# Performance work log

Hardware: AMD Instinct MI355X
Metric: run time of the kernel (lower is better)

The kernel has to match this reference:

```python
import jax, jax.numpy as jnp
import numpy as np

B, L, D = 2, 2048, 1024
H = 16
HD = D // H  # 64


def _orthogonal_projection(key, d, m):
    g = jax.random.normal(key, (d, m), dtype=jnp.float32)
    q, r = jnp.linalg.qr(g)
    s = jnp.sign(jnp.diagonal(r))
    s = jnp.where(s == 0, 1.0, s)
    q = q * s[None, :]
    # preserve_variance=True
    return q * np.sqrt(d / m)


def setup_inputs() -> dict:
    key = jax.random.key(0)
    ks = jax.random.split(key, 8)
    x = jax.random.normal(ks[0], (B, L, D), dtype=jnp.float32)
    p = jax.random.normal(ks[1], (B, L, D), dtype=jnp.float32)
    s = 1.0 / np.sqrt(D)
    W_qkv = jax.random.uniform(ks[2], (3 * D, D), dtype=jnp.float32, minval=-s, maxval=s)
    b_qkv = jax.random.uniform(ks[3], (3 * D,), dtype=jnp.float32, minval=-s, maxval=s)
    W_out = jax.random.uniform(ks[4], (D, D), dtype=jnp.float32, minval=-s, maxval=s)
    b_out = jax.random.uniform(ks[5], (D,), dtype=jnp.float32, minval=-s, maxval=s)
    proj = _orthogonal_projection(ks[6], D, D // 2)
    return {"x": x, "p": p, "W_qkv": W_qkv, "b_qkv": b_qkv,
            "W_out": W_out, "b_out": b_out, "proj": proj}


def reference(x, p, W_qkv, b_qkv, W_out, b_out, proj):
    # QKV projection: (B,L,D) -> (B,L,3,H,HD)
    qkv = (jnp.einsum('bld,ed->ble', x, W_qkv) + b_qkv).reshape(B, L, 3, H, HD)
    q, k, v = qkv[:, :, 0], qkv[:, :, 1], qkv[:, :, 2]

    # Collaborative rotary phases from conditioning tokens: (B,L,H,HD/2)
    phases = (p @ proj).reshape(B, L, H, HD // 2)  # phase_scale = 1.0
    cos, sin = jnp.cos(phases), jnp.sin(phases)

    half = HD // 2
    # non-interleaved rotary: split head_dim into two halves
    def rot(t):
        t1, t2 = t[..., :half], t[..., half:]
        return jnp.concatenate([t1 * cos - t2 * sin, t1 * sin + t2 * cos], axis=-1)

    q, k = rot(q), rot(k)

    scale = HD ** -0.5
    scores = jnp.einsum('bqhd,bkhd->bhqk', q, k) * scale
    attn = jax.nn.softmax(scores, axis=-1)
    out = jnp.einsum('bhqk,bkhd->bqhd', attn, v).reshape(B, L, D)
    return jnp.einsum('bld,ed->ble', out, W_out) + b_out
```

## Files before the change

kernel.cpp:

```cpp
#include <hip/hip_runtime.h>
#include <hip/hip_bf16.h>
#include <math.h>

namespace {
constexpr int Bb = 2;
constexpr int Ll = 2048;
constexpr int Dd = 1024;
constexpr int Hh = 16;
constexpr int NT = Bb * Ll;
constexpr int D3 = 3 * Dd;
constexpr int PH = Dd / 2;
constexpr int LDK = 72;
}

typedef __attribute__((ext_vector_type(8))) short bf16x8;
typedef __attribute__((ext_vector_type(4))) short bf16x4;
typedef __attribute__((ext_vector_type(4))) float f32x4;

#if defined(__has_builtin)
#if __has_builtin(__builtin_amdgcn_mfma_f32_16x16x16bf16_1k)
#define HAVE_MFMA16 1
#endif
#endif

__device__ inline unsigned pack2bf(float a, float b) {
  __hip_bfloat162 t = __float22bfloat162_rn(float2{a, b});
  union { __hip_bfloat162 h; unsigned u; } cv; cv.h = t;
  return cv.u;
}

__device__ inline bf16x4 u2bf4(uint2 u) {
  union { uint2 u; bf16x4 v; } c; c.u = u; return c.v;
}

__device__ inline f32x4 pv_mfma(bf16x4 va, bf16x4 vb, f32x4 c) {
#ifdef HAVE_MFMA16
  return __builtin_amdgcn_mfma_f32_16x16x16bf16_1k(va, vb, c, 0, 0, 0);
#else
  const bf16x8 a8 = {va[0], va[1], va[2], va[3], 0, 0, 0, 0};
  const bf16x8 b8 = {vb[0], vb[1], vb[2], vb[3], 0, 0, 0, 0};
  return __builtin_amdgcn_mfma_f32_16x16x32_bf16(a8, b8, c, 0, 0, 0);
#endif
}

__device__ inline void async_cp16(const void* gsrc, void* ldst) {
  __builtin_amdgcn_global_load_lds(
      (const __attribute__((address_space(1))) unsigned int*)gsrc,
      (__attribute__((address_space(3))) unsigned int*)ldst, 16, 0, 0);
}

__global__ __launch_bounds__(256) void cast3_kernel(
    const float4* __restrict__ x, const float4* __restrict__ wq,
    const float4* __restrict__ wo,
    uint2* __restrict__ xd, uint2* __restrict__ wqd, uint2* __restrict__ wod)
{
  int i = blockIdx.x * 256 + threadIdx.x;
  const float4* s; uint2* d;
  if (i < 1048576) { s = x; d = xd; }
  else if (i < 1048576 + 786432) { i -= 1048576; s = wq; d = wqd; }
  else { i -= 1048576 + 786432; s = wo; d = wod; }
  const float4 f = s[i];
  d[i] = make_uint2(pack2bf(f.x, f.y), pack2bf(f.z, f.w));
}

__global__ __launch_bounds__(256) void split_cast_kernel(
    const float4* __restrict__ src, uint2* __restrict__ hi, uint2* __restrict__ lo, int n4)
{
  const int i = blockIdx.x * 256 + threadIdx.x;
  if (i >= n4) return;
  const float4 f = src[i];
  float hf[4], lf[4];
  const float ff[4] = {f.x, f.y, f.z, f.w};
#pragma unroll
  for (int j = 0; j < 4; ++j) {
    const __hip_bfloat16 h = __float2bfloat16(ff[j]);
    hf[j] = __bfloat162float(h);
    lf[j] = ff[j] - hf[j];
  }
  hi[i] = make_uint2(pack2bf(hf[0], hf[1]), pack2bf(hf[2], hf[3]));
  lo[i] = make_uint2(pack2bf(lf[0], lf[1]), pack2bf(lf[2], lf[3]));
}

__global__ __launch_bounds__(256) void trans_split_kernel(
    const float* __restrict__ proj, short* __restrict__ th, short* __restrict__ tl)
{
  __shared__ float Ls[64][65];
  const int tid = threadIdx.x;
  const int d0 = blockIdx.x * 64, m0 = blockIdx.y * 64;
  const int r = tid >> 4, c4 = (tid & 15) * 4;
#pragma unroll
  for (int it = 0; it < 4; ++it) {
    const int row = it * 16 + r;
    const float4 v = *(const float4*)&proj[(size_t)(d0 + row) * PH + m0 + c4];
    Ls[row][c4] = v.x; Ls[row][c4+1] = v.y; Ls[row][c4+2] = v.z; Ls[row][c4+3] = v.w;
  }
  __syncthreads();
#pragma unroll
  for (int it = 0; it < 4; ++it) {
    const int row = it * 16 + r;
    float hf[4], lf[4];
#pragma unroll
    for (int j = 0; j < 4; ++j) {
      const float v = Ls[c4 + j][row];
      const __hip_bfloat16 h = __float2bfloat16(v);
      hf[j] = __bfloat162float(h);
      lf[j] = v - hf[j];
    }
    *(uint2*)&th[(size_t)(m0 + row) * Dd + d0 + c4] = make_uint2(pack2bf(hf[0], hf[1]), pack2bf(hf[2], hf[3]));
    *(uint2*)&tl[(size_t)(m0 + row) * Dd + d0 + c4] = make_uint2(pack2bf(lf[0], lf[1]), pack2bf(lf[2], lf[3]));
  }
}

__global__ __launch_bounds__(256) void gemm_nn_split(
    const short* __restrict__ Ah_g, const short* __restrict__ Al_g,
    const short* __restrict__ Wh_g, const short* __restrict__ Wl_g,
    float* __restrict__ C)
{
  __shared__ __align__(16) short Ah[64 * 32], Al[64 * 32], Wh[64 * 32], Wl[64 * 32];
  const int tid = threadIdx.x;
  const int w = tid >> 6, lane = tid & 63;
  const int l15 = lane & 15, quad = lane >> 4;
  const int wn = w >> 1, wm = w & 1;
  const int n0 = blockIdx.y * 64, m0 = blockIdx.x * 64;

  const int row = tid >> 2, cc = tid & 3;
  const int ksw = (cc ^ (row & 3)) * 8;
  const short* gAh = Ah_g + (size_t)(n0 + row) * Dd + ksw;
  const short* gAl = Al_g + (size_t)(n0 + row) * Dd + ksw;
  const short* gWh = Wh_g + (size_t)(m0 + row) * Dd + ksw;
  const short* gWl = Wl_g + (size_t)(m0 + row) * Dd + ksw;
  short* lAh = Ah + tid * 8;
  short* lAl = Al + tid * 8;
  short* lWh = Wh + tid * 8;
  short* lWl = Wl + tid * 8;

  f32x4 acc[2][2];
#pragma unroll
  for (int i = 0; i < 2; ++i)
#pragma unroll
    for (int j = 0; j < 2; ++j) acc[i][j] = f32x4{0.f, 0.f, 0.f, 0.f};

  const int swq = (quad ^ (l15 & 3)) * 8;

  for (int k0 = 0; k0 < Dd; k0 += 32) {
    __syncthreads();
    async_cp16(gAh + k0, lAh);
    async_cp16(gAl + k0, lAl);
    async_cp16(gWh + k0, lWh);
    async_cp16(gWl + k0, lWl);
    __syncthreads();

    bf16x8 ah[2], al[2], wh[2], wl[2];
#pragma unroll
    for (int i = 0; i < 2; ++i) {
      ah[i] = *(const bf16x8*)&Ah[(wn * 32 + i * 16 + l15) * 32 + swq];
      al[i] = *(const bf16x8*)&Al[(wn * 32 + i * 16 + l15) * 32 + swq];
    }
#pragma unroll
    for (int j = 0; j < 2; ++j) {
      wh[j] = *(const bf16x8*)&Wh[(wm * 32 + j * 16 + l15) * 32 + swq];
      wl[j] = *(const bf16x8*)&Wl[(wm * 32 + j * 16 + l15) * 32 + swq];
    }
#pragma unroll
    for (int i = 0; i < 2; ++i)
#pragma unroll
      for (int j = 0; j < 2; ++j) {
        acc[i][j] = __builtin_amdgcn_mfma_f32_16x16x32_bf16(ah[i], wh[j], acc[i][j], 0, 0, 0);
        acc[i][j] = __builtin_amdgcn_mfma_f32_16x16x32_bf16(ah[i], wl[j], acc[i][j], 0, 0, 0);
        acc[i][j] = __builtin_amdgcn_mfma_f32_16x16x32_bf16(al[i], wh[j], acc[i][j], 0, 0, 0);
      }
  }

#pragma unroll
  for (int i = 0; i < 2; ++i)
#pragma unroll
    for (int r = 0; r < 4; ++r) {
      float* crow = C + (size_t)(n0 + wn * 32 + i * 16 + quad * 4 + r) * PH + m0 + wm * 32 + l15;
#pragma unroll
      for (int j = 0; j < 2; ++j) crow[j * 16] = acc[i][j][r];
    }
}

__global__ __launch_bounds__(256) void gemm_qkv_fused(
    const __hip_bfloat16* __restrict__ A, const __hip_bfloat16* __restrict__ W,
    const float* __restrict__ bias, const float* __restrict__ phases,
    __hip_bfloat16* __restrict__ q_bf, __hip_bfloat16* __restrict__ k_bf,
    __hip_bfloat16* __restrict__ vt_g)
{
  __shared__ __align__(16) short As[128 * 32];
  __shared__ __align__(16) short Ws[128 * 32];
  const int tid = threadIdx.x;
  const int w = tid >> 6, lane = tid & 63;
  const int l15 = lane & 15, quad = lane >> 4;
  const int wn = w >> 1, wm = w & 1;
  const int n0 = blockIdx.y * 128, m0 = blockIdx.x * 128;

  const int row = tid >> 2, cc = tid & 3;
  const int ksw = (cc ^ (row & 3)) * 8;
  const short* gA  = (const short*)A + (size_t)(n0 + row) * Dd + ksw;
  const short* gW  = (const short*)W + (size_t)(m0 + row) * Dd + ksw;
  short* lA  = As + tid * 8;
  short* lA2 = As + 2048 + tid * 8;
  short* lW  = Ws + tid * 8;
  short* lW2 = Ws + 2048 + tid * 8;

  f32x4 acc[4][4];
#pragma unroll
  for (int i = 0; i < 4; ++i)
#pragma unroll
    for (int j = 0; j < 4; ++j) acc[i][j] = f32x4{0.f, 0.f, 0.f, 0.f};

  const int swq = (quad ^ (l15 & 3)) * 8;

  for (int k0 = 0; k0 < Dd; k0 += 32) {
    __syncthreads();
    async_cp16(gA + k0, lA);
    async_cp16(gA + 64 * Dd + k0, lA2);
    async_cp16(gW + k0, lW);
    async_cp16(gW + 64 * Dd + k0, lW2);
    __syncthreads();

    bf16x8 af[4], bf[4];
#pragma unroll
    for (int i = 0; i < 4; ++i)
      af[i] = *(const bf16x8*)&As[(wn * 64 + i * 16 + l15) * 32 + swq];
#pragma unroll
    for (int j = 0; j < 4; ++j)
      bf[j] = *(const bf16x8*)&Ws[(wm * 64 + j * 16 + l15) * 32 + swq];
#pragma unroll
    for (int i = 0; i < 4; ++i)
#pragma unroll
      for (int j = 0; j < 4; ++j)
        acc[i][j] = __builtin_amdgcn_mfma_f32_16x16x32_bf16(af[i], bf[j], acc[i][j], 0, 0, 0);
  }

  float bv[4];
#pragma unroll
  for (int j = 0; j < 4; ++j) bv[j] = bias[m0 + wm * 64 + j * 16 + l15];

  const int region = m0 >> 10;
  const int mloc = (m0 & 1023) + wm * 64;
  const int h = mloc >> 6;

  if (region < 2) {
    __hip_bfloat16* dst = region == 0 ? q_bf : k_bf;
    const float SC = region == 0 ? 0.18033688011112042f : 1.0f;
#pragma unroll
    for (int i = 0; i < 4; ++i)
#pragma unroll
      for (int r = 0; r < 4; ++r) {
        const int n = n0 + wn * 64 + i * 16 + quad * 4 + r;
        const float* phrow = phases + (size_t)n * PH + h * 32;
        __hip_bfloat16* drow = dst + (size_t)n * Dd + h * 64;
#pragma unroll
        for (int pz = 0; pz < 2; ++pz) {
          const float ph = phrow[pz * 16 + l15];
          float sn, cs;
          __sincosf(ph, &sn, &cs);
          const float a1 = acc[i][pz][r] + bv[pz];
          const float a2 = acc[i][pz + 2][r] + bv[pz + 2];
          drow[pz * 16 + l15]      = __float2bfloat16((a1 * cs - a2 * sn) * SC);
          drow[pz * 16 + 32 + l15] = __float2bfloat16((a1 * sn + a2 * cs) * SC);
        }
      }
  } else {
    const int bh = (n0 >> 11) * 16 + h;
    const int tokb = (n0 & 2047) + wn * 64;
#pragma unroll
    for (int i = 0; i < 4; ++i)
#pragma unroll
      for (int j = 0; j < 4; ++j) {
        const uint2 o = make_uint2(
            pack2bf(acc[i][j][0] + bv[j], acc[i][j][1] + bv[j]),
            pack2bf(acc[i][j][2] + bv[j], acc[i][j][3] + bv[j]));
        const int d = j * 16 + l15;
        *(uint2*)&vt_g[(size_t)(bh * 64 + d) * Ll + tokb + i * 16 + quad * 4] = o;
      }
  }
}

__global__ __launch_bounds__(256) void gemm_bt_bf16(
    const __hip_bfloat16* __restrict__ A, const __hip_bfloat16* __restrict__ W,
    const float* __restrict__ bias, float* __restrict__ C, int K, int M)
{
  __shared__ __align__(16) short As[128 * 32];
  __shared__ __align__(16) short Ws[128 * 32];
  const int tid = threadIdx.x;
  const int w = tid >> 6, lane = tid & 63;
  const int l15 = lane & 15, quad = lane >> 4;
  const int wn = w >> 1, wm = w & 1;
  const int n0 = blockIdx.y * 128, m0 = blockIdx.x * 128;

  const int row = tid >> 2, cc = tid & 3;
  const int ksw = (cc ^ (row & 3)) * 8;
  const short* gA  = (const short*)A + (size_t)(n0 + row) * K + ksw;
  const short* gW  = (const short*)W + (size_t)(m0 + row) * K + ksw;
  short* lA  = As + tid * 8;
  short* lA2 = As + 2048 + tid * 8;
  short* lW  = Ws + tid * 8;
  short* lW2 = Ws + 2048 + tid * 8;

  f32x4 acc[4][4];
#pragma unroll
  for (int i = 0; i < 4; ++i)
#pragma unroll
    for (int j = 0; j < 4; ++j) acc[i][j] = f32x4{0.f, 0.f, 0.f, 0.f};

  const int swq = (quad ^ (l15 & 3)) * 8;

  for (int k0 = 0; k0 < K; k0 += 32) {
    __syncthreads();
    async_cp16(gA + k0, lA);
    async_cp16(gA + 64 * K + k0, lA2);
    async_cp16(gW + k0, lW);
    async_cp16(gW + 64 * K + k0, lW2);
    __syncthreads();

    bf16x8 af[4], bf[4];
#pragma unroll
    for (int i = 0; i < 4; ++i)
      af[i] = *(const bf16x8*)&As[(wn * 64 + i * 16 + l15) * 32 + swq];
#pragma unroll
    for (int j = 0; j < 4; ++j)
      bf[j] = *(const bf16x8*)&Ws[(wm * 64 + j * 16 + l15) * 32 + swq];
#pragma unroll
    for (int i = 0; i < 4; ++i)
#pragma unroll
      for (int j = 0; j < 4; ++j)
        acc[i][j] = __builtin_amdgcn_mfma_f32_16x16x32_bf16(af[i], bf[j], acc[i][j], 0, 0, 0);
  }

  float bv[4];
#pragma unroll
  for (int j = 0; j < 4; ++j) bv[j] = bias[m0 + wm * 64 + j * 16 + l15];
#pragma unroll
  for (int i = 0; i < 4; ++i)
#pragma unroll
    for (int r = 0; r < 4; ++r) {
      float* crow = C + (size_t)(n0 + wn * 64 + i * 16 + quad * 4 + r) * M + m0 + wm * 64 + l15;
#pragma unroll
      for (int j = 0; j < 4; ++j) crow[j * 16] = acc[i][j][r] + bv[j];
    }
}

__global__ __launch_bounds__(256) void attn_mfma(
    const __hip_bfloat16* __restrict__ q_bf,
    const __hip_bfloat16* __restrict__ k_bf,
    const __hip_bfloat16* __restrict__ vt_g,
    __hip_bfloat16* __restrict__ aout)
{
  __shared__ __align__(16) short Ks[64 * LDK];
  __shared__ __align__(16) short Vt[64 * LDK];

  const int tid = threadIdx.x;
  const int w = tid >> 6;
  const int lane = tid & 63;
  const int l15 = lane & 15;
  const int quad = lane >> 4;

  const int q0 = blockIdx.x * 128;
  const int bh = blockIdx.y;
  const int b = bh >> 4, h = bh & 15;

  bf16x8 qfrag[2][2];
#pragma unroll
  for (int qg = 0; qg < 2; ++qg)
#pragma unroll
    for (int kh = 0; kh < 2; ++kh) {
      const size_t qrow = (size_t)(b * Ll + q0 + w * 32 + qg * 16 + l15);
      qfrag[qg][kh] = *(const bf16x8*)(q_bf + qrow * Dd + h * 64 + kh * 32 + quad * 8);
    }

  f32x4 acc[4][2];
#pragma unroll
  for (int dt = 0; dt < 4; ++dt)
#pragma unroll
    for (int qg = 0; qg < 2; ++qg) acc[dt][qg] = f32x4{0.f, 0.f, 0.f, 0.f};
  float l_acc[2] = {0.f, 0.f};

  const int srow = tid >> 2, sseg = tid & 3;
  const __hip_bfloat16* kbase = k_bf + (size_t)(b * Ll + srow) * Dd + h * 64 + sseg * 16;
  const __hip_bfloat16* vbase = vt_g + ((size_t)(bh * 64 + srow)) * Ll + sseg * 16;

  for (int kt = 0; kt < Ll / 64; ++kt) {
    __syncthreads();
    {
      const uint4* kg = (const uint4*)(kbase + (size_t)kt * 64 * Dd);
      *(uint4*)&Ks[srow * LDK + sseg * 16]     = kg[0];
      *(uint4*)&Ks[srow * LDK + sseg * 16 + 8] = kg[1];
      const uint4* vg = (const uint4*)(vbase + kt * 64);
      *(uint4*)&Vt[srow * LDK + sseg * 16]     = vg[0];
      *(uint4*)&Vt[srow * LDK + sseg * 16 + 8] = vg[1];
    }
    __syncthreads();

    f32x4 s[4][2];
#pragma unroll
    for (int n = 0; n < 4; ++n)
#pragma unroll
      for (int qg = 0; qg < 2; ++qg) s[n][qg] = f32x4{0.f, 0.f, 0.f, 0.f};
#pragma unroll
    for (int n = 0; n < 4; ++n)
#pragma unroll
      for (int kh = 0; kh < 2; ++kh) {
        const bf16x8 af = *(const bf16x8*)&Ks[(n * 16 + l15) * LDK + kh * 32 + quad * 8];
        s[n][0] = __builtin_amdgcn_mfma_f32_16x16x32_bf16(af, qfrag[0][kh], s[n][0], 0, 0, 0);
        s[n][1] = __builtin_amdgcn_mfma_f32_16x16x32_bf16(af, qfrag[1][kh], s[n][1], 0, 0, 0);
      }

    uint2 bq[4][2];
#pragma unroll
    for (int qg = 0; qg < 2; ++qg)
#pragma unroll
      for (int n = 0; n < 4; ++n) {
        union { float f; unsigned u; } p0, p1, p2, p3, t0, t1, t2, t3;
        p0.f = __builtin_amdgcn_exp2f(s[n][qg][0]);
        p1.f = __builtin_amdgcn_exp2f(s[n][qg][1]);
        p2.f = __builtin_amdgcn_exp2f(s[n][qg][2]);
        p3.f = __builtin_amdgcn_exp2f(s[n][qg][3]);
        const unsigned lo = __builtin_amdgcn_perm(p1.u, p0.u, 0x07060302u);
        const unsigned hi = __builtin_amdgcn_perm(p3.u, p2.u, 0x07060302u);
        bq[n][qg] = make_uint2(lo, hi);
        t0.u = lo << 16; t1.u = lo & 0xffff0000u;
        t2.u = hi << 16; t3.u = hi & 0xffff0000u;
        l_acc[qg] += (t0.f + t1.f) + (t2.f + t3.f);
      }

#pragma unroll
    for (int n = 0; n < 4; ++n) {
      const bf16x4 pb0 = u2bf4(bq[n][0]);
      const bf16x4 pb1 = u2bf4(bq[n][1]);
#pragma unroll
      for (int dt = 0; dt < 4; ++dt) {
        const bf16x4 va = *(const bf16x4*)&Vt[(dt * 16 + l15) * LDK + n * 16 + quad * 4];
        acc[dt][0] = pv_mfma(va, pb0, acc[dt][0]);
        acc[dt][1] = pv_mfma(va, pb1, acc[dt][1]);
      }
    }
  }

#pragma unroll
  for (int qg = 0; qg < 2; ++qg) {
    float l = l_acc[qg];
    l += __shfl_xor(l, 16);
    l += __shfl_xor(l, 32);
    const float linv = 1.f / l;
    const size_t q = (size_t)(b * Ll + q0 + w * 32 + qg * 16 + l15);
#pragma unroll
    for (int dt = 0; dt < 4; ++dt) {
      const uint2 o = make_uint2(
          pack2bf(acc[dt][qg][0] * linv, acc[dt][qg][1] * linv),
          pack2bf(acc[dt][qg][2] * linv, acc[dt][qg][3] * linv));
      *(uint2*)&aout[q * Dd + h * 64 + dt * 16 + quad * 4] = o;
    }
  }
}

extern "C" void kernel_launch(void* const* d_in, const int* in_sizes, int n_in,
                              void* d_out, int out_size, void* d_ws, size_t ws_size,
                              hipStream_t stream) {
  const float* x     = (const float*)d_in[0];
  const float* p     = (const float*)d_in[1];
  const float* W_qkv = (const float*)d_in[2];
  const float* b_qkv = (const float*)d_in[3];
  const float* W_out = (const float*)d_in[4];
  const float* b_out = (const float*)d_in[5];
  const float* proj  = (const float*)d_in[6];
  float* out = (float*)d_out;

  char* wsb = (char*)d_ws;
  float*          phases   = (float*)(wsb);
  short*          p_hi     = (short*)(wsb + (8u << 20));
  __hip_bfloat16* aout_bf  = (__hip_bfloat16*)(wsb + (8u << 20));
  short*          p_lo     = (short*)(wsb + (16u << 20));
  __hip_bfloat16* vt_g     = (__hip_bfloat16*)(wsb + (16u << 20));
  short*          projt_hi = (short*)(wsb + (24u << 20));
  short*          projt_lo = (short*)(wsb + (25u << 20));
  __hip_bfloat16* q_bf     = (__hip_bfloat16*)(wsb + (26u << 20));
  __hip_bfloat16* k_bf     = (__hip_bfloat16*)(wsb + (34u << 20));
  __hip_bfloat16* x_bf     = (__hip_bfloat16*)(wsb + (42u << 20));
  __hip_bfloat16* wqkv_bf  = (__hip_bfloat16*)(wsb + (50u << 20));
  __hip_bfloat16* wout_bf  = (__hip_bfloat16*)(wsb + (56u << 20));

  split_cast_kernel<<<4096, 256, 0, stream>>>((const float4*)p, (uint2*)p_hi, (uint2*)p_lo, 1048576);
  trans_split_kernel<<<dim3(Dd / 64, PH / 64), 256, 0, stream>>>(proj, projt_hi, projt_lo);
  cast3_kernel<<<8192, 256, 0, stream>>>((const float4*)x, (const float4*)W_qkv, (const float4*)W_out,
                                         (uint2*)x_bf, (uint2*)wqkv_bf, (uint2*)wout_bf);
  gemm_nn_split<<<dim3(PH / 64, NT / 64), 256, 0, stream>>>(p_hi, p_lo, projt_hi, projt_lo, phases);
  gemm_qkv_fused<<<dim3(D3 / 128, NT / 128), 256, 0, stream>>>(x_bf, wqkv_bf, b_qkv, phases,
                                                               q_bf, k_bf, vt_g);
  attn_mfma<<<dim3(Ll / 128, Bb * Hh), 256, 0, stream>>>(q_bf, k_bf, vt_g, aout_bf);
  gemm_bt_bf16<<<dim3(Dd / 128, NT / 128), 256, 0, stream>>>(aout_bf, wout_bf, b_out, out, Dd, Dd);
}
```

Before: 275.1 us.

## Enlarge phase GEMM tile, prefetch K/V into registers, compute softmax denominator via MFMA

```diff
diff --git a/kernel.cpp b/kernel.cpp
--- a/kernel.cpp
+++ b/kernel.cpp
@@ -116,12 +116,11 @@
     const short* __restrict__ Wh_g, const short* __restrict__ Wl_g,
     float* __restrict__ C)
 {
-  __shared__ __align__(16) short Ah[64 * 32], Al[64 * 32], Wh[64 * 32], Wl[64 * 32];
+  __shared__ __align__(16) short Ah[128 * 32], Al[128 * 32], Wh[64 * 32], Wl[64 * 32];
   const int tid = threadIdx.x;
   const int w = tid >> 6, lane = tid & 63;
   const int l15 = lane & 15, quad = lane >> 4;
-  const int wn = w >> 1, wm = w & 1;
-  const int n0 = blockIdx.y * 64, m0 = blockIdx.x * 64;
+  const int n0 = blockIdx.y * 128, m0 = blockIdx.x * 64;
 
   const int row = tid >> 2, cc = tid & 3;
   const int ksw = (cc ^ (row & 3)) * 8;
@@ -129,42 +128,46 @@
   const short* gAl = Al_g + (size_t)(n0 + row) * Dd + ksw;
   const short* gWh = Wh_g + (size_t)(m0 + row) * Dd + ksw;
   const short* gWl = Wl_g + (size_t)(m0 + row) * Dd + ksw;
-  short* lAh = Ah + tid * 8;
-  short* lAl = Al + tid * 8;
-  short* lWh = Wh + tid * 8;
-  short* lWl = Wl + tid * 8;
-
-  f32x4 acc[2][2];
+  short* lAh  = Ah + tid * 8;
+  short* lAh2 = Ah + 2048 + tid * 8;
+  short* lAl  = Al + tid * 8;
+  short* lAl2 = Al + 2048 + tid * 8;
+  short* lWh  = Wh + tid * 8;
+  short* lWl  = Wl + tid * 8;
+
+  f32x4 acc[2][4];
 #pragma unroll
   for (int i = 0; i < 2; ++i)
 #pragma unroll
-    for (int j = 0; j < 2; ++j) acc[i][j] = f32x4{0.f, 0.f, 0.f, 0.f};
+    for (int j = 0; j < 4; ++j) acc[i][j] = f32x4{0.f, 0.f, 0.f, 0.f};
 
   const int swq = (quad ^ (l15 & 3)) * 8;
 
   for (int k0 = 0; k0 < Dd; k0 += 32) {
     __syncthreads();
     async_cp16(gAh + k0, lAh);
+    async_cp16(gAh + 64 * Dd + k0, lAh2);
     async_cp16(gAl + k0, lAl);
+    async_cp16(gAl + 64 * Dd + k0, lAl2);
     async_cp16(gWh + k0, lWh);
     async_cp16(gWl + k0, lWl);
     __syncthreads();
 
-    bf16x8 ah[2], al[2], wh[2], wl[2];
+    bf16x8 ah[2], al[2], wh[4], wl[4];
 #pragma unroll
     for (int i = 0; i < 2; ++i) {
-      ah[i] = *(const bf16x8*)&Ah[(wn * 32 + i * 16 + l15) * 32 + swq];
-      al[i] = *(const bf16x8*)&Al[(wn * 32 + i * 16 + l15) * 32 + swq];
-    }
-#pragma unroll
-    for (int j = 0; j < 2; ++j) {
-      wh[j] = *(const bf16x8*)&Wh[(wm * 32 + j * 16 + l15) * 32 + swq];
-      wl[j] = *(const bf16x8*)&Wl[(wm * 32 + j * 16 + l15) * 32 + swq];
+      ah[i] = *(const bf16x8*)&Ah[(w * 32 + i * 16 + l15) * 32 + swq];
+      al[i] = *(const bf16x8*)&Al[(w * 32 + i * 16 + l15) * 32 + swq];
+    }
+#pragma unroll
+    for (int j = 0; j < 4; ++j) {
+      wh[j] = *(const bf16x8*)&Wh[(j * 16 + l15) * 32 + swq];
+      wl[j] = *(const bf16x8*)&Wl[(j * 16 + l15) * 32 + swq];
     }
 #pragma unroll
     for (int i = 0; i < 2; ++i)
 #pragma unroll
-      for (int j = 0; j < 2; ++j) {
+      for (int j = 0; j < 4; ++j) {
         acc[i][j] = __builtin_amdgcn_mfma_f32_16x16x32_bf16(ah[i], wh[j], acc[i][j], 0, 0, 0);
         acc[i][j] = __builtin_amdgcn_mfma_f32_16x16x32_bf16(ah[i], wl[j], acc[i][j], 0, 0, 0);
         acc[i][j] = __builtin_amdgcn_mfma_f32_16x16x32_bf16(al[i], wh[j], acc[i][j], 0, 0, 0);
@@ -175,9 +178,9 @@
   for (int i = 0; i < 2; ++i)
 #pragma unroll
     for (int r = 0; r < 4; ++r) {
-      float* crow = C + (size_t)(n0 + wn * 32 + i * 16 + quad * 4 + r) * PH + m0 + wm * 32 + l15;
-#pragma unroll
-      for (int j = 0; j < 2; ++j) crow[j * 16] = acc[i][j][r];
+      float* crow = C + (size_t)(n0 + w * 32 + i * 16 + quad * 4 + r) * PH + m0 + l15;
+#pragma unroll
+      for (int j = 0; j < 4; ++j) crow[j * 16] = acc[i][j][r];
     }
 }
 
@@ -376,23 +379,37 @@
   for (int dt = 0; dt < 4; ++dt)
 #pragma unroll
     for (int qg = 0; qg < 2; ++qg) acc[dt][qg] = f32x4{0.f, 0.f, 0.f, 0.f};
-  float l_acc[2] = {0.f, 0.f};
+  f32x4 lden[2] = {f32x4{0.f,0.f,0.f,0.f}, f32x4{0.f,0.f,0.f,0.f}};
+  const short one_bf = (short)0x3F80;
+  const bf16x4 ones = {one_bf, one_bf, one_bf, one_bf};
 
   const int srow = tid >> 2, sseg = tid & 3;
   const __hip_bfloat16* kbase = k_bf + (size_t)(b * Ll + srow) * Dd + h * 64 + sseg * 16;
   const __hip_bfloat16* vbase = vt_g + ((size_t)(bh * 64 + srow)) * Ll + sseg * 16;
 
+  uint4 pk0, pk1, pv0, pv1;
+  {
+    const uint4* kg = (const uint4*)kbase;
+    pk0 = kg[0]; pk1 = kg[1];
+    const uint4* vg = (const uint4*)vbase;
+    pv0 = vg[0]; pv1 = vg[1];
+  }
+
   for (int kt = 0; kt < Ll / 64; ++kt) {
     __syncthreads();
+    *(uint4*)&Ks[srow * LDK + sseg * 16]     = pk0;
+    *(uint4*)&Ks[srow * LDK + sseg * 16 + 8] = pk1;
+    *(uint4*)&Vt[srow * LDK + sseg * 16]     = pv0;
+    *(uint4*)&Vt[srow * LDK + sseg * 16 + 8] = pv1;
+    __syncthreads();
+
     {
-      const uint4* kg = (const uint4*)(kbase + (size_t)kt * 64 * Dd);
-      *(uint4*)&Ks[srow * LDK + sseg * 16]     = kg[0];
-      *(uint4*)&Ks[srow * LDK + sseg * 16 + 8] = kg[1];
-      const uint4* vg = (const uint4*)(vbase + kt * 64);
-      *(uint4*)&Vt[srow * LDK + sseg * 16]     = vg[0];
-      *(uint4*)&Vt[srow * LDK + sseg * 16 + 8] = vg[1];
-    }
-    __syncthreads();
+      const int ktn = (kt + 1) & 31;
+      const uint4* kg = (const uint4*)(kbase + (size_t)ktn * 64 * Dd);
+      pk0 = kg[0]; pk1 = kg[1];
+      const uint4* vg = (const uint4*)(vbase + ktn * 64);
+      pv0 = vg[0]; pv1 = vg[1];
+    }
 
     f32x4 s[4][2];
 #pragma unroll
@@ -413,23 +430,21 @@
     for (int qg = 0; qg < 2; ++qg)
 #pragma unroll
       for (int n = 0; n < 4; ++n) {
-        union { float f; unsigned u; } p0, p1, p2, p3, t0, t1, t2, t3;
+        union { float f; unsigned u; } p0, p1, p2, p3;
         p0.f = __builtin_amdgcn_exp2f(s[n][qg][0]);
         p1.f = __builtin_amdgcn_exp2f(s[n][qg][1]);
         p2.f = __builtin_amdgcn_exp2f(s[n][qg][2]);
         p3.f = __builtin_amdgcn_exp2f(s[n][qg][3]);
-        const unsigned lo = __builtin_amdgcn_perm(p1.u, p0.u, 0x07060302u);
-        const unsigned hi = __builtin_amdgcn_perm(p3.u, p2.u, 0x07060302u);
-        bq[n][qg] = make_uint2(lo, hi);
-        t0.u = lo << 16; t1.u = lo & 0xffff0000u;
-        t2.u = hi << 16; t3.u = hi & 0xffff0000u;
-        l_acc[qg] += (t0.f + t1.f) + (t2.f + t3.f);
+        bq[n][qg] = make_uint2(__builtin_amdgcn_perm(p1.u, p0.u, 0x07060302u),
+                               __builtin_amdgcn_perm(p3.u, p2.u, 0x07060302u));
       }
 
 #pragma unroll
     for (int n = 0; n < 4; ++n) {
       const bf16x4 pb0 = u2bf4(bq[n][0]);
       const bf16x4 pb1 = u2bf4(bq[n][1]);
+      lden[0] = pv_mfma(ones, pb0, lden[0]);
+      lden[1] = pv_mfma(ones, pb1, lden[1]);
 #pragma unroll
       for (int dt = 0; dt < 4; ++dt) {
         const bf16x4 va = *(const bf16x4*)&Vt[(dt * 16 + l15) * LDK + n * 16 + quad * 4];
@@ -441,10 +456,7 @@
 
 #pragma unroll
   for (int qg = 0; qg < 2; ++qg) {
-    float l = l_acc[qg];
-    l += __shfl_xor(l, 16);
-    l += __shfl_xor(l, 32);
-    const float linv = 1.f / l;
+    const float linv = 1.f / lden[qg][0];
     const size_t q = (size_t)(b * Ll + q0 + w * 32 + qg * 16 + l15);
 #pragma unroll
     for (int dt = 0; dt < 4; ++dt) {
@@ -486,7 +498,7 @@
   trans_split_kernel<<<dim3(Dd / 64, PH / 64), 256, 0, stream>>>(proj, projt_hi, projt_lo);
   cast3_kernel<<<8192, 256, 0, stream>>>((const float4*)x, (const float4*)W_qkv, (const float4*)W_out,
                                          (uint2*)x_bf, (uint2*)wqkv_bf, (uint2*)wout_bf);
-  gemm_nn_split<<<dim3(PH / 64, NT / 64), 256, 0, stream>>>(p_hi, p_lo, projt_hi, projt_lo, phases);
+  gemm_nn_split<<<dim3(PH / 64, NT / 128), 256, 0, stream>>>(p_hi, p_lo, projt_hi, projt_lo, phases);
   gemm_qkv_fused<<<dim3(D3 / 128, NT / 128), 256, 0, stream>>>(x_bf, wqkv_bf, b_qkv, phases,
                                                                q_bf, k_bf, vt_g);
   attn_mfma<<<dim3(Ll / 128, Bb * Hh), 256, 0, stream>>>(q_bf, k_bf, vt_g, aout_bf);
```

Measured after the change: 269.3 us. -2.1%, faster.
